# Kernel optimization log

Measured on AMD Instinct MI355X. Metric: run time of the kernel, lower is better.

The kernel has to match this reference:

```python
import math
import jax, jax.numpy as jnp
import numpy as np
from jax import lax

UP = 2
DOWN = 2
M = 8
BETA = 2.5
FC = 0.5          # up_fc = down_fc = 0.5 (not 'critical' branch)
LRELU = 0.1

def _lpf_filter(factor):
    # Kaiser-windowed sinc, matches Resampler.__init__ (fc != 'critical' branch)
    Mf = M * factor
    n = np.arange(-Mf // 2, Mf // 2 + 1).astype(np.float32)   # 17 taps
    cutoff = FC * math.pi
    f = np.sin(cutoff * n) / (math.pi * n + 1e-8)
    f[len(n) // 2] = FC
    win = np.kaiser(Mf + 1, BETA).astype(np.float32)          # == torch.kaiser_window(.., periodic=False)
    return jnp.asarray(win * f, dtype=jnp.float32)

UP_FILT = _lpf_filter(UP)
DOWN_FILT = _lpf_filter(DOWN)

def _conv1d_same(x, w, groups=1):
    # x: (B, Cin, L), w: (Cout, Cin//groups, K) with odd K
    pad = (w.shape[-1] - 1) // 2
    return lax.conv_general_dilated(x, w, window_strides=(1,), padding=[(pad, pad)],
                                    dimension_numbers=('NCH', 'OIH', 'NCH'),
                                    feature_group_count=groups)

def _lpf(x, filt):
    # depthwise grouped FIR, padding='same'
    C = x.shape[1]
    f = jnp.broadcast_to(filt[None, None, :], (C, 1, filt.shape[0]))
    return _conv1d_same(x, f, groups=C)

def setup_inputs() -> dict:
    key = jax.random.key(0)
    ks = jax.random.split(key, 4)
    bs, c_in, c_out, w_dim, L, k = 16, 512, 512, 512, 2048, 3
    return {
        'x': jax.random.normal(ks[0], (bs, c_in, L), dtype=jnp.float32),
        'w': jax.random.normal(ks[1], (bs, w_dim), dtype=jnp.float32),
        'affine_w': jax.random.normal(ks[2], (c_in, w_dim), dtype=jnp.float32) * 0.02,
        'affine_b': jnp.ones((c_in,), dtype=jnp.float32),
        'conv_w': jax.random.normal(ks[3], (c_out, c_in, k), dtype=jnp.float32) * 0.05,
        'conv_b': jnp.zeros((c_out,), dtype=jnp.float32),
        'norm_ema': jnp.ones((), dtype=jnp.float32),
    }

def reference(x, w, affine_w, affine_b, conv_w, conv_b, norm_ema):
    # eval mode, equalized_lr=False, normalize=True
    x = x * lax.rsqrt(norm_ema)
    cond = w @ affine_w.T + affine_b                                      # (bs, c_in)
    # weight / style normalization
    Wn = conv_w * lax.rsqrt(jnp.mean(jnp.square(conv_w), axis=(1, 2), keepdims=True))
    s = cond * lax.rsqrt(jnp.mean(jnp.square(cond)))                      # (bs, c_in)
    # demod coeff: rsqrt(sum_{i,k} (Wn[o,i,k]*s[b,i])^2 + 1e-8)
    d = lax.rsqrt(jnp.einsum('oik,bi->bo', jnp.square(Wn), jnp.square(s)) + 1e-8)
    # modulate-conv-demodulate (equivalent to per-sample grouped conv with conv_w[None]*s*d)
    y = _conv1d_same(x * s[:, :, None], Wn) * d[:, :, None] + conv_b[None, :, None]
    # upsample: zero-insertion then interpolation LPF
    bs, C, L = y.shape
    y = jnp.pad(y[..., None], ((0, 0), (0, 0), (0, 0), (0, UP - 1))).reshape(bs, C, L * UP)
    y = _lpf(y, UP_FILT)
    # filtered nonlinearity
    y = jax.nn.leaky_relu(y, LRELU) * math.sqrt(2)
    # downsample: anti-alias LPF then decimate
    y = _lpf(y, DOWN_FILT)[:, :, ::DOWN]
    return y
```

## Files before the change

### kernel.cpp

```cpp
#include <hip/hip_runtime.h>
#include <cmath>

typedef __attribute__((ext_vector_type(8))) short short8;
typedef __attribute__((ext_vector_type(4))) float f32x4;

static __device__ __forceinline__ unsigned short f2bf(float x) {
  unsigned int u = __float_as_uint(x);
  unsigned int r = (u + 0x7FFFu + ((u >> 16) & 1u)) >> 16;
  return (unsigned short)r;
}
static __device__ __forceinline__ float bf2f(unsigned short u) {
  return __uint_as_float(((unsigned int)u) << 16);
}
static __device__ __forceinline__ void glds16(const unsigned short* g, unsigned short* l) {
  __builtin_amdgcn_global_load_lds((const __attribute__((address_space(1))) unsigned int*)(g),
                                   (__attribute__((address_space(3))) unsigned int*)(l), 16, 0, 0);
}

__global__ __launch_bounds__(256) void k_cond(const float* __restrict__ w,
    const float* __restrict__ aw, const float* __restrict__ ab,
    float* __restrict__ cond, float* __restrict__ ssum) {
  int t = threadIdx.x;
  int outp = blockIdx.x * 64 + (t >> 2);
  int sub = t & 3;
  int b = outp >> 9, i = outp & 511;
  const float4* wr = (const float4*)(w + b * 512);
  const float4* ar = (const float4*)(aw + i * 512);
  float acc = 0.f;
  #pragma unroll
  for (int jj = 0; jj < 32; ++jj) {
    int j = sub + jj * 4;
    float4 a = ar[j], v = wr[j];
    acc += a.x * v.x + a.y * v.y + a.z * v.z + a.w * v.w;
  }
  acc += __shfl_xor(acc, 1);
  acc += __shfl_xor(acc, 2);
  float s = 0.f;
  if (sub == 0) {
    float c = acc + ab[i];
    cond[outp] = c;
    s = c * c;
  }
  #pragma unroll
  for (int off = 4; off <= 32; off <<= 1) s += __shfl_xor(s, off);
  if ((t & 63) == 0) atomicAdd(ssum, s);
}

__global__ __launch_bounds__(256) void k_wprep(const float* __restrict__ cw,
    float* __restrict__ W2, float* __restrict__ rinv,
    unsigned short* __restrict__ wpack) {
  int o = blockIdx.x, t = threadIdx.x;
  const float* row = cw + o * 1536;
  __shared__ float red[4];
  float local = 0.f;
  for (int r = 0; r < 2; ++r) {
    int i = t + 256 * r;
    float a = row[3 * i], b = row[3 * i + 1], c = row[3 * i + 2];
    float w2 = a * a + b * b + c * c;
    W2[o * 512 + i] = w2;
    local += w2;
    int chunk = i >> 5;
    int laneo = (((i >> 3) & 3) << 4) + (o & 15);
    int e = i & 7;
    int base = (chunk * 32 + (o >> 4)) * 512 + laneo * 8 + e;
    wpack[base] = f2bf(a);
    wpack[base + 16 * 32 * 512] = f2bf(b);
    wpack[base + 2 * 16 * 32 * 512] = f2bf(c);
  }
  #pragma unroll
  for (int off = 32; off >= 1; off >>= 1) local += __shfl_down(local, off);
  if ((t & 63) == 0) red[t >> 6] = local;
  __syncthreads();
  if (t == 0) {
    float m = red[0] + red[1] + red[2] + red[3];
    rinv[o] = rsqrtf(m * (1.f / 1536.f));
  }
}

__global__ __launch_bounds__(256) void k_dcoef(const float* __restrict__ W2,
    const float* __restrict__ cond, const float* __restrict__ rinv,
    const float* __restrict__ ssum, float* __restrict__ coef) {
  int og = blockIdx.x, b = blockIdx.y;
  int t = threadIdx.x;
  int o = og * 32 + (t >> 3);
  int il = t & 7;
  __shared__ float s2[512];
  float c0 = cond[b * 512 + t];
  float c1 = cond[b * 512 + t + 256];
  s2[t] = c0 * c0;
  s2[t + 256] = c1 * c1;
  __syncthreads();
  float acc = 0.f;
  #pragma unroll
  for (int jj = 0; jj < 16; ++jj) {
    int i = jj * 32 + il * 4;
    float4 wv = *(const float4*)(W2 + o * 512 + i);
    acc += wv.x * s2[i] + wv.y * s2[i + 1] + wv.z * s2[i + 2] + wv.w * s2[i + 3];
  }
  acc += __shfl_xor(acc, 1);
  acc += __shfl_xor(acc, 2);
  acc += __shfl_xor(acc, 4);
  if (il == 0) {
    float inv_ms = 8192.f / ssum[0];
    float ro = rinv[o];
    coef[b * 512 + o] = ro * rsqrtf(ro * ro * acc * inv_ms + 1e-8f);
  }
}

__global__ __launch_bounds__(256) void k_xprep(const float* __restrict__ x,
    const float* __restrict__ cond, const float* __restrict__ ssum,
    const float* __restrict__ nrm, unsigned short* __restrict__ xsT) {
  int lb = blockIdx.x, ib = blockIdx.y, b = blockIdx.z;
  int t = threadIdx.x;
  int l0 = lb * 64, i0 = ib * 64;
  __shared__ float tile[64][65];
  float sc = rsqrtf(ssum[0] * (1.f / 8192.f)) * rsqrtf(nrm[0]);
  int tr = t >> 4, tc = (t & 15) * 4;
  #pragma unroll
  for (int rr = 0; rr < 4; ++rr) {
    int il = rr * 16 + tr;
    float se = cond[b * 512 + i0 + il] * sc;
    float4 v = *(const float4*)(x + ((size_t)b * 512 + i0 + il) * 2048 + l0 + tc);
    tile[il][tc + 0] = v.x * se;
    tile[il][tc + 1] = v.y * se;
    tile[il][tc + 2] = v.z * se;
    tile[il][tc + 3] = v.w * se;
  }
  __syncthreads();
  int lr = t >> 3, ic = (t & 7) * 8;
  #pragma unroll
  for (int rr = 0; rr < 2; ++rr) {
    int ll = rr * 32 + lr;
    uint4 u;
    unsigned int pk[4];
    #pragma unroll
    for (int j = 0; j < 4; ++j) {
      unsigned short lo = f2bf(tile[ic + 2 * j][ll]);
      unsigned short hi = f2bf(tile[ic + 2 * j + 1][ll]);
      pk[j] = (unsigned int)lo | ((unsigned int)hi << 16);
    }
    u.x = pk[0]; u.y = pk[1]; u.z = pk[2]; u.w = pk[3];
    *(uint4*)(xsT + ((size_t)b * 2050 + 1 + l0 + ll) * 512 + i0 + ic) = u;
  }
  if (lb == 0 && t < 8) {
    uint4 z; z.x = 0; z.y = 0; z.z = 0; z.w = 0;
    *(uint4*)(xsT + ((size_t)b * 2050) * 512 + i0 + t * 8) = z;
  }
  if (lb == 31 && t < 8) {
    uint4 z; z.x = 0; z.y = 0; z.z = 0; z.w = 0;
    *(uint4*)(xsT + ((size_t)b * 2050 + 2049) * 512 + i0 + t * 8) = z;
  }
}

#define STAGE_B(buf, c) { \
  _Pragma("unroll") for (int j_ = 0; j_ < 3; ++j_) { \
    int f_ = j_ * 256 + t; \
    if (f_ < 520) { \
      int col_ = ((f_ >> 3) << 1) | (((f_ >> 2) ^ (f_ >> 4)) & 1); \
      int q_ = ((f_ ^ (f_ >> 2) ^ (f_ >> 4)) & 1) | ((((f_ >> 1) ^ (f_ >> 3)) & 1) << 1); \
      const unsigned short* src_ = xsT + ((size_t)b * 2050 + l0 + col_) * 512 + (c) * 32 + q_ * 8; \
      glds16(src_, &Bl[buf][(f_ & ~63) * 8]); \
    } \
  } }

#define LOAD_A(Ar, c) { \
  _Pragma("unroll") for (int k_ = 0; k_ < 3; ++k_) \
  _Pragma("unroll") for (int rg_ = 0; rg_ < 4; ++rg_) \
    Ar[k_ * 4 + rg_] = *(const short8*)(wpack + ((size_t)((k_ * 16 + (c)) * 32 + ob * 8 + wr * 4 + rg_)) * 512 + lane * 8); }

#define MFMA_STEP(Ar, buf) { \
  _Pragma("unroll") for (int k_ = 0; k_ < 3; ++k_) { \
    short8 bfr_[4]; \
    _Pragma("unroll") for (int cg_ = 0; cg_ < 4; ++cg_) { \
      int col_ = wc * 64 + cg_ * 16 + (lane & 15) + k_; \
      int byte_ = (col_ * 64 + ((lane >> 4) << 4)) ^ ((col_ & 7) << 4); \
      bfr_[cg_] = *(const short8*)((const char*)Bl[buf] + byte_); \
    } \
    _Pragma("unroll") for (int rg_ = 0; rg_ < 4; ++rg_) \
      _Pragma("unroll") for (int cg_ = 0; cg_ < 4; ++cg_) \
        acc[rg_][cg_] = __builtin_amdgcn_mfma_f32_16x16x32_bf16(Ar[k_ * 4 + rg_], bfr_[cg_], acc[rg_][cg_], 0, 0, 0); \
  } }

__global__ __launch_bounds__(256, 2) void k_main(const unsigned short* __restrict__ xsT,
    const unsigned short* __restrict__ wpack, const float* __restrict__ coef,
    const float* __restrict__ convb, unsigned short* __restrict__ y) {
  int lb = blockIdx.x, ob = blockIdx.y, b = blockIdx.z;
  int t = threadIdx.x, lane = t & 63, wave = t >> 6;
  int wr = wave >> 1, wc = wave & 1;
  int l0 = lb * 128, o0 = ob * 128;
  __shared__ __align__(16) unsigned short Bl[2][4160];
  f32x4 acc[4][4];
  f32x4 z4 = {0.f, 0.f, 0.f, 0.f};
  #pragma unroll
  for (int i = 0; i < 4; ++i)
    #pragma unroll
    for (int j = 0; j < 4; ++j) acc[i][j] = z4;

  short8 A0[12], A1[12];
  LOAD_A(A0, 0);
  STAGE_B(0, 0);
  __syncthreads();
  for (int cc = 0; cc < 16; cc += 2) {
    if (cc + 1 < 16) { STAGE_B(1, cc + 1); LOAD_A(A1, cc + 1); }
    MFMA_STEP(A0, 0);
    __syncthreads();
    if (cc + 2 < 16) { STAGE_B(0, cc + 2); LOAD_A(A0, cc + 2); }
    MFMA_STEP(A1, 1);
    __syncthreads();
  }
  int lq = lane >> 4, lrr = lane & 15;
  #pragma unroll
  for (int rg = 0; rg < 4; ++rg) {
    int o2 = o0 + wr * 64 + rg * 16 + lq * 4;
    float c0 = coef[b * 512 + o2 + 0], c1 = coef[b * 512 + o2 + 1];
    float c2 = coef[b * 512 + o2 + 2], c3 = coef[b * 512 + o2 + 3];
    float b0 = convb[o2 + 0], b1 = convb[o2 + 1];
    float b2 = convb[o2 + 2], b3 = convb[o2 + 3];
    #pragma unroll
    for (int cg = 0; cg < 4; ++cg) {
      int l = l0 + wc * 64 + cg * 16 + lrr;
      y[((size_t)b * 512 + o2 + 0) * 4096 + l] = f2bf(acc[rg][cg][0] * c0 + b0);
      y[((size_t)b * 512 + o2 + 1) * 4096 + l] = f2bf(acc[rg][cg][1] * c1 + b1);
      y[((size_t)b * 512 + o2 + 2) * 4096 + l] = f2bf(acc[rg][cg][2] * c2 + b2);
      y[((size_t)b * 512 + o2 + 3) * 4096 + l] = f2bf(acc[rg][cg][3] * c3 + b3);
    }
  }
}

struct Taps { float f[8]; };

__global__ __launch_bounds__(256) void k_filter(const unsigned short* __restrict__ ybuf,
    float* __restrict__ out, Taps tp) {
  int ch = blockIdx.x;
  int t = threadIdx.x;
  __shared__ float ysb[2336];
  const unsigned short* yc = ybuf + (size_t)ch * 4096;
  uint4 v = *(const uint4*)(yc + 8 * t);
  unsigned int wsv[4] = {v.x, v.y, v.z, v.w};
  int phys0 = 9 * t + 9;
  #pragma unroll
  for (int p = 0; p < 4; ++p) {
    ysb[phys0 + 2 * p]     = bf2f((unsigned short)(wsv[p] & 0xffffu));
    ysb[phys0 + 2 * p + 1] = bf2f((unsigned short)(wsv[p] >> 16));
  }
  if (t < 8) ysb[t] = 0.f;
  if (t >= 240 && t < 255) {
    int j = 2056 + (t - 240);
    ysb[j + (j >> 3)] = 0.f;
  }
  __syncthreads();
  float r[22];
  int jb = 8 * t + 1;
  #pragma unroll
  for (int u = 0; u < 22; ++u) { int j = jb + u; r[u] = ysb[j + (j >> 3)]; }
  int m0 = 8 * t;
  float ao[15];
  #pragma unroll
  for (int vv = 0; vv < 15; ++vv) {
    int t4 = m0 - 4 + vv;
    float u = 0.f;
    #pragma unroll
    for (int p = 0; p < 8; ++p) u += tp.f[p] * r[vv + p];
    float a = (u >= 0.f ? u : 0.1f * u) * 1.41421356237309515f;
    ao[vv] = ((unsigned)t4 < 2048u) ? a : 0.f;
  }
  float res[8];
  #pragma unroll
  for (int w = 0; w < 8; ++w) {
    float yv = r[w + 7];
    float s = 0.35355339059327379f * (yv >= 0.f ? yv : 0.1f * yv);
    #pragma unroll
    for (int q = 0; q < 8; ++q) s += tp.f[q] * ao[w + q];
    res[w] = s;
  }
  float4 o0; o0.x = res[0]; o0.y = res[1]; o0.z = res[2]; o0.w = res[3];
  float4 o1; o1.x = res[4]; o1.y = res[5]; o1.z = res[6]; o1.w = res[7];
  float* orow = out + (size_t)ch * 2048 + m0;
  *(float4*)orow = o0;
  *((float4*)orow + 1) = o1;
}

static double bessel_i0(double x) {
  double s = 1.0, term = 1.0;
  for (int m = 1; m < 30; ++m) {
    double h = x * 0.5 / (double)m;
    term *= h * h;
    s += term;
  }
  return s;
}

extern "C" void kernel_launch(void* const* d_in, const int* in_sizes, int n_in,
                              void* d_out, int out_size, void* d_ws, size_t ws_size,
                              hipStream_t stream) {
  (void)in_sizes; (void)n_in; (void)out_size; (void)ws_size;
  const float* x  = (const float*)d_in[0];
  const float* w  = (const float*)d_in[1];
  const float* aw = (const float*)d_in[2];
  const float* ab = (const float*)d_in[3];
  const float* cw = (const float*)d_in[4];
  const float* cb = (const float*)d_in[5];
  const float* ne = (const float*)d_in[6];
  float* out = (float*)d_out;
  char* ws = (char*)d_ws;

  float* ssum = (float*)(ws + 0);
  float* cond = (float*)(ws + 4096);
  float* coef = (float*)(ws + 36864);
  float* rinv = (float*)(ws + 69632);
  unsigned short* wpack = (unsigned short*)(ws + 73728);
  float* W2 = (float*)(ws + 3219456);
  unsigned short* xsT = (unsigned short*)(ws + 4268032);

  hipMemsetAsync(ssum, 0, 4, stream);
  k_cond<<<128, 256, 0, stream>>>(w, aw, ab, cond, ssum);
  k_wprep<<<512, 256, 0, stream>>>(cw, W2, rinv, wpack);
  k_dcoef<<<dim3(16, 16), 256, 0, stream>>>(W2, cond, rinv, ssum, coef);
  k_xprep<<<dim3(32, 8, 16), 256, 0, stream>>>(x, cond, ssum, ne, xsT);
  k_main<<<dim3(16, 4, 16), 256, 0, stream>>>(xsT, wpack, coef, cb, (unsigned short*)d_out);

  Taps tp;
  {
    double beta = 2.5;
    double i0b = bessel_i0(beta);
    for (int p = 0; p < 8; ++p) {
      int j = 2 * p + 1;
      int n = j - 8;
      double f = sin(0.5 * M_PI * (double)n) / (M_PI * (double)n + 1e-8);
      double rr = (double)(j - 8) / 8.0;
      double win = bessel_i0(beta * sqrt(1.0 - rr * rr)) / i0b;
      tp.f[p] = (float)(win * f);
    }
  }
  k_filter<<<8192, 256, 0, stream>>>((const unsigned short*)d_out, out, tp);
}
```

Measured before the change: 208.4 us.

## Triple-buffer main GEMM with vmcnt waits and merge prep kernels

Merges the four preprocessing kernels into two launches by dispatching on block index, which cuts launch overhead and serialization between them. The main MFMA kernel moves from double to triple buffering of the B tile in LDS. It uses explicit vmcnt waits and raw s_barrier instead of __syncthreads, so loads run two chunks ahead. Staging is now assigned per wave and the occupancy hint rises to 3 blocks per CU. In exchange it uses more LDS and depends on hand-counted vmcnt values, which risks races if the counts are wrong.

```diff
diff --git a/kernel.cpp b/kernel.cpp
--- a/kernel.cpp
+++ b/kernel.cpp
@@ -17,149 +17,151 @@
                                    (__attribute__((address_space(3))) unsigned int*)(l), 16, 0, 0);
 }
 
-__global__ __launch_bounds__(256) void k_cond(const float* __restrict__ w,
+#define VWAIT(n) asm volatile("s_waitcnt vmcnt(" #n ")" ::: "memory")
+
+__global__ __launch_bounds__(256) void k_pre1(const float* __restrict__ w,
     const float* __restrict__ aw, const float* __restrict__ ab,
-    float* __restrict__ cond, float* __restrict__ ssum) {
-  int t = threadIdx.x;
-  int outp = blockIdx.x * 64 + (t >> 2);
-  int sub = t & 3;
-  int b = outp >> 9, i = outp & 511;
-  const float4* wr = (const float4*)(w + b * 512);
-  const float4* ar = (const float4*)(aw + i * 512);
-  float acc = 0.f;
-  #pragma unroll
-  for (int jj = 0; jj < 32; ++jj) {
-    int j = sub + jj * 4;
-    float4 a = ar[j], v = wr[j];
-    acc += a.x * v.x + a.y * v.y + a.z * v.z + a.w * v.w;
-  }
-  acc += __shfl_xor(acc, 1);
-  acc += __shfl_xor(acc, 2);
-  float s = 0.f;
-  if (sub == 0) {
-    float c = acc + ab[i];
-    cond[outp] = c;
-    s = c * c;
-  }
-  #pragma unroll
-  for (int off = 4; off <= 32; off <<= 1) s += __shfl_xor(s, off);
-  if ((t & 63) == 0) atomicAdd(ssum, s);
-}
-
-__global__ __launch_bounds__(256) void k_wprep(const float* __restrict__ cw,
-    float* __restrict__ W2, float* __restrict__ rinv,
-    unsigned short* __restrict__ wpack) {
-  int o = blockIdx.x, t = threadIdx.x;
-  const float* row = cw + o * 1536;
+    const float* __restrict__ cw, float* __restrict__ cond, float* __restrict__ ssum,
+    float* __restrict__ W2, float* __restrict__ rinv, unsigned short* __restrict__ wpack) {
   __shared__ float red[4];
-  float local = 0.f;
-  for (int r = 0; r < 2; ++r) {
-    int i = t + 256 * r;
-    float a = row[3 * i], b = row[3 * i + 1], c = row[3 * i + 2];
-    float w2 = a * a + b * b + c * c;
-    W2[o * 512 + i] = w2;
-    local += w2;
-    int chunk = i >> 5;
-    int laneo = (((i >> 3) & 3) << 4) + (o & 15);
-    int e = i & 7;
-    int base = (chunk * 32 + (o >> 4)) * 512 + laneo * 8 + e;
-    wpack[base] = f2bf(a);
-    wpack[base + 16 * 32 * 512] = f2bf(b);
-    wpack[base + 2 * 16 * 32 * 512] = f2bf(c);
-  }
-  #pragma unroll
-  for (int off = 32; off >= 1; off >>= 1) local += __shfl_down(local, off);
-  if ((t & 63) == 0) red[t >> 6] = local;
-  __syncthreads();
-  if (t == 0) {
-    float m = red[0] + red[1] + red[2] + red[3];
-    rinv[o] = rsqrtf(m * (1.f / 1536.f));
-  }
-}
-
-__global__ __launch_bounds__(256) void k_dcoef(const float* __restrict__ W2,
-    const float* __restrict__ cond, const float* __restrict__ rinv,
-    const float* __restrict__ ssum, float* __restrict__ coef) {
-  int og = blockIdx.x, b = blockIdx.y;
-  int t = threadIdx.x;
-  int o = og * 32 + (t >> 3);
-  int il = t & 7;
-  __shared__ float s2[512];
-  float c0 = cond[b * 512 + t];
-  float c1 = cond[b * 512 + t + 256];
-  s2[t] = c0 * c0;
-  s2[t + 256] = c1 * c1;
-  __syncthreads();
-  float acc = 0.f;
-  #pragma unroll
-  for (int jj = 0; jj < 16; ++jj) {
-    int i = jj * 32 + il * 4;
-    float4 wv = *(const float4*)(W2 + o * 512 + i);
-    acc += wv.x * s2[i] + wv.y * s2[i + 1] + wv.z * s2[i + 2] + wv.w * s2[i + 3];
-  }
-  acc += __shfl_xor(acc, 1);
-  acc += __shfl_xor(acc, 2);
-  acc += __shfl_xor(acc, 4);
-  if (il == 0) {
-    float inv_ms = 8192.f / ssum[0];
-    float ro = rinv[o];
-    coef[b * 512 + o] = ro * rsqrtf(ro * ro * acc * inv_ms + 1e-8f);
-  }
-}
-
-__global__ __launch_bounds__(256) void k_xprep(const float* __restrict__ x,
-    const float* __restrict__ cond, const float* __restrict__ ssum,
-    const float* __restrict__ nrm, unsigned short* __restrict__ xsT) {
-  int lb = blockIdx.x, ib = blockIdx.y, b = blockIdx.z;
-  int t = threadIdx.x;
-  int l0 = lb * 64, i0 = ib * 64;
-  __shared__ float tile[64][65];
-  float sc = rsqrtf(ssum[0] * (1.f / 8192.f)) * rsqrtf(nrm[0]);
-  int tr = t >> 4, tc = (t & 15) * 4;
-  #pragma unroll
-  for (int rr = 0; rr < 4; ++rr) {
-    int il = rr * 16 + tr;
-    float se = cond[b * 512 + i0 + il] * sc;
-    float4 v = *(const float4*)(x + ((size_t)b * 512 + i0 + il) * 2048 + l0 + tc);
-    tile[il][tc + 0] = v.x * se;
-    tile[il][tc + 1] = v.y * se;
-    tile[il][tc + 2] = v.z * se;
-    tile[il][tc + 3] = v.w * se;
-  }
-  __syncthreads();
-  int lr = t >> 3, ic = (t & 7) * 8;
-  #pragma unroll
-  for (int rr = 0; rr < 2; ++rr) {
-    int ll = rr * 32 + lr;
-    uint4 u;
-    unsigned int pk[4];
-    #pragma unroll
-    for (int j = 0; j < 4; ++j) {
-      unsigned short lo = f2bf(tile[ic + 2 * j][ll]);
-      unsigned short hi = f2bf(tile[ic + 2 * j + 1][ll]);
-      pk[j] = (unsigned int)lo | ((unsigned int)hi << 16);
-    }
-    u.x = pk[0]; u.y = pk[1]; u.z = pk[2]; u.w = pk[3];
-    *(uint4*)(xsT + ((size_t)b * 2050 + 1 + l0 + ll) * 512 + i0 + ic) = u;
-  }
-  if (lb == 0 && t < 8) {
-    uint4 z; z.x = 0; z.y = 0; z.z = 0; z.w = 0;
-    *(uint4*)(xsT + ((size_t)b * 2050) * 512 + i0 + t * 8) = z;
-  }
-  if (lb == 31 && t < 8) {
-    uint4 z; z.x = 0; z.y = 0; z.z = 0; z.w = 0;
-    *(uint4*)(xsT + ((size_t)b * 2050 + 2049) * 512 + i0 + t * 8) = z;
+  int bid = blockIdx.x, t = threadIdx.x;
+  if (bid < 128) {
+    int outp = bid * 64 + (t >> 2);
+    int sub = t & 3;
+    int b = outp >> 9, i = outp & 511;
+    const float4* wr = (const float4*)(w + b * 512);
+    const float4* ar = (const float4*)(aw + i * 512);
+    float acc = 0.f;
+    #pragma unroll
+    for (int jj = 0; jj < 32; ++jj) {
+      int j = sub + jj * 4;
+      float4 a = ar[j], v = wr[j];
+      acc += a.x * v.x + a.y * v.y + a.z * v.z + a.w * v.w;
+    }
+    acc += __shfl_xor(acc, 1);
+    acc += __shfl_xor(acc, 2);
+    float s = 0.f;
+    if (sub == 0) {
+      float c = acc + ab[i];
+      cond[outp] = c;
+      s = c * c;
+    }
+    #pragma unroll
+    for (int off = 4; off <= 32; off <<= 1) s += __shfl_xor(s, off);
+    if ((t & 63) == 0) atomicAdd(ssum, s);
+  } else {
+    int o = bid - 128;
+    const float* row = cw + o * 1536;
+    float local = 0.f;
+    for (int r = 0; r < 2; ++r) {
+      int i = t + 256 * r;
+      float a = row[3 * i], b = row[3 * i + 1], c = row[3 * i + 2];
+      float w2 = a * a + b * b + c * c;
+      W2[o * 512 + i] = w2;
+      local += w2;
+      int chunk = i >> 5;
+      int laneo = (((i >> 3) & 3) << 4) + (o & 15);
+      int e = i & 7;
+      int base = (chunk * 32 + (o >> 4)) * 512 + laneo * 8 + e;
+      wpack[base] = f2bf(a);
+      wpack[base + 16 * 32 * 512] = f2bf(b);
+      wpack[base + 2 * 16 * 32 * 512] = f2bf(c);
+    }
+    #pragma unroll
+    for (int off = 32; off >= 1; off >>= 1) local += __shfl_down(local, off);
+    if ((t & 63) == 0) red[t >> 6] = local;
+    __syncthreads();
+    if (t == 0) {
+      float m = red[0] + red[1] + red[2] + red[3];
+      rinv[o] = rsqrtf(m * (1.f / 1536.f));
+    }
+  }
+}
+
+__global__ __launch_bounds__(256) void k_pre2(const float* __restrict__ x,
+    const float* __restrict__ W2, const float* __restrict__ cond,
+    const float* __restrict__ rinv, const float* __restrict__ ssum,
+    const float* __restrict__ nrm, float* __restrict__ coef,
+    unsigned short* __restrict__ xsT) {
+  __shared__ float shb[64 * 65];
+  int bid = blockIdx.x, t = threadIdx.x;
+  if (bid < 256) {
+    int og = bid & 15, b = bid >> 4;
+    int o = og * 32 + (t >> 3);
+    int il = t & 7;
+    float c0 = cond[b * 512 + t];
+    float c1 = cond[b * 512 + t + 256];
+    shb[t] = c0 * c0;
+    shb[t + 256] = c1 * c1;
+    __syncthreads();
+    float acc = 0.f;
+    #pragma unroll
+    for (int jj = 0; jj < 16; ++jj) {
+      int i = jj * 32 + il * 4;
+      float4 wv = *(const float4*)(W2 + o * 512 + i);
+      acc += wv.x * shb[i] + wv.y * shb[i + 1] + wv.z * shb[i + 2] + wv.w * shb[i + 3];
+    }
+    acc += __shfl_xor(acc, 1);
+    acc += __shfl_xor(acc, 2);
+    acc += __shfl_xor(acc, 4);
+    if (il == 0) {
+      float inv_ms = 8192.f / ssum[0];
+      float ro = rinv[o];
+      coef[b * 512 + o] = ro * rsqrtf(ro * ro * acc * inv_ms + 1e-8f);
+    }
+  } else {
+    int xb = bid - 256;
+    int lb = xb & 31, ib = (xb >> 5) & 7, b = xb >> 8;
+    float (*tile)[65] = (float(*)[65])shb;
+    int l0 = lb * 64, i0 = ib * 64;
+    float sc = rsqrtf(ssum[0] * (1.f / 8192.f)) * rsqrtf(nrm[0]);
+    int tr = t >> 4, tc = (t & 15) * 4;
+    #pragma unroll
+    for (int rr = 0; rr < 4; ++rr) {
+      int il = rr * 16 + tr;
+      float se = cond[b * 512 + i0 + il] * sc;
+      float4 v = *(const float4*)(x + ((size_t)b * 512 + i0 + il) * 2048 + l0 + tc);
+      tile[il][tc + 0] = v.x * se;
+      tile[il][tc + 1] = v.y * se;
+      tile[il][tc + 2] = v.z * se;
+      tile[il][tc + 3] = v.w * se;
+    }
+    __syncthreads();
+    int lr = t >> 3, ic = (t & 7) * 8;
+    #pragma unroll
+    for (int rr = 0; rr < 2; ++rr) {
+      int ll = rr * 32 + lr;
+      uint4 u;
+      unsigned int pk[4];
+      #pragma unroll
+      for (int j = 0; j < 4; ++j) {
+        unsigned short lo = f2bf(tile[ic + 2 * j][ll]);
+        unsigned short hi = f2bf(tile[ic + 2 * j + 1][ll]);
+        pk[j] = (unsigned int)lo | ((unsigned int)hi << 16);
+      }
+      u.x = pk[0]; u.y = pk[1]; u.z = pk[2]; u.w = pk[3];
+      *(uint4*)(xsT + ((size_t)b * 2050 + 1 + l0 + ll) * 512 + i0 + ic) = u;
+    }
+    if (lb == 0 && t < 8) {
+      uint4 z; z.x = 0; z.y = 0; z.z = 0; z.w = 0;
+      *(uint4*)(xsT + ((size_t)b * 2050) * 512 + i0 + t * 8) = z;
+    }
+    if (lb == 31 && t < 8) {
+      uint4 z; z.x = 0; z.y = 0; z.z = 0; z.w = 0;
+      *(uint4*)(xsT + ((size_t)b * 2050 + 2049) * 512 + i0 + t * 8) = z;
+    }
   }
 }
 
 #define STAGE_B(buf, c) { \
   _Pragma("unroll") for (int j_ = 0; j_ < 3; ++j_) { \
-    int f_ = j_ * 256 + t; \
-    if (f_ < 520) { \
-      int col_ = ((f_ >> 3) << 1) | (((f_ >> 2) ^ (f_ >> 4)) & 1); \
-      int q_ = ((f_ ^ (f_ >> 2) ^ (f_ >> 4)) & 1) | ((((f_ >> 1) ^ (f_ >> 3)) & 1) << 1); \
+    int sb_ = wave * 130 + ((j_ < 2) ? j_ * 64 : 128); \
+    int s_ = sb_ + ((j_ < 2) ? lane : (lane & 1)); \
+    if (j_ < 2 || lane < 2) { \
+      int col_ = ((s_ >> 3) << 1) | (((s_ >> 2) ^ (s_ >> 4)) & 1); \
+      int q_ = ((s_ ^ (s_ >> 2) ^ (s_ >> 4)) & 1) | ((((s_ >> 1) ^ (s_ >> 3)) & 1) << 1); \
       const unsigned short* src_ = xsT + ((size_t)b * 2050 + l0 + col_) * 512 + (c) * 32 + q_ * 8; \
-      glds16(src_, &Bl[buf][(f_ & ~63) * 8]); \
+      glds16(src_, &Bl[buf][sb_ * 8]); \
     } \
   } }
 
@@ -181,14 +183,14 @@
         acc[rg_][cg_] = __builtin_amdgcn_mfma_f32_16x16x32_bf16(Ar[k_ * 4 + rg_], bfr_[cg_], acc[rg_][cg_], 0, 0, 0); \
   } }
 
-__global__ __launch_bounds__(256, 2) void k_main(const unsigned short* __restrict__ xsT,
+__global__ __launch_bounds__(256, 3) void k_main(const unsigned short* __restrict__ xsT,
     const unsigned short* __restrict__ wpack, const float* __restrict__ coef,
     const float* __restrict__ convb, unsigned short* __restrict__ y) {
   int lb = blockIdx.x, ob = blockIdx.y, b = blockIdx.z;
   int t = threadIdx.x, lane = t & 63, wave = t >> 6;
   int wr = wave >> 1, wc = wave & 1;
   int l0 = lb * 128, o0 = ob * 128;
-  __shared__ __align__(16) unsigned short Bl[2][4160];
+  __shared__ __align__(16) unsigned short Bl[3][4160];
   f32x4 acc[4][4];
   f32x4 z4 = {0.f, 0.f, 0.f, 0.f};
   #pragma unroll
@@ -196,18 +198,32 @@
     #pragma unroll
     for (int j = 0; j < 4; ++j) acc[i][j] = z4;
 
-  short8 A0[12], A1[12];
-  LOAD_A(A0, 0);
+  short8 Areg[2][12];
+  LOAD_A(Areg[0], 0);
   STAGE_B(0, 0);
-  __syncthreads();
-  for (int cc = 0; cc < 16; cc += 2) {
-    if (cc + 1 < 16) { STAGE_B(1, cc + 1); LOAD_A(A1, cc + 1); }
-    MFMA_STEP(A0, 0);
-    __syncthreads();
-    if (cc + 2 < 16) { STAGE_B(0, cc + 2); LOAD_A(A0, cc + 2); }
-    MFMA_STEP(A1, 1);
-    __syncthreads();
-  }
+  STAGE_B(1, 1);
+  __builtin_amdgcn_sched_barrier(0);
+  VWAIT(3);
+  __builtin_amdgcn_s_barrier();
+
+  #pragma unroll
+  for (int c = 0; c < 14; ++c) {
+    LOAD_A(Areg[(c + 1) & 1], c + 1);
+    STAGE_B((c + 2) % 3, c + 2);
+    __builtin_amdgcn_sched_barrier(0);
+    MFMA_STEP(Areg[c & 1], c % 3);
+    __builtin_amdgcn_sched_barrier(0);
+    VWAIT(15);
+    __builtin_amdgcn_s_barrier();
+  }
+  LOAD_A(Areg[1], 15);
+  __builtin_amdgcn_sched_barrier(0);
+  MFMA_STEP(Areg[0], 2);
+  __builtin_amdgcn_sched_barrier(0);
+  VWAIT(12);
+  __builtin_amdgcn_s_barrier();
+  MFMA_STEP(Areg[1], 0);
+
   int lq = lane >> 4, lrr = lane & 15;
   #pragma unroll
   for (int rg = 0; rg < 4; ++rg) {
@@ -313,10 +329,8 @@
   unsigned short* xsT = (unsigned short*)(ws + 4268032);
 
   hipMemsetAsync(ssum, 0, 4, stream);
-  k_cond<<<128, 256, 0, stream>>>(w, aw, ab, cond, ssum);
-  k_wprep<<<512, 256, 0, stream>>>(cw, W2, rinv, wpack);
-  k_dcoef<<<dim3(16, 16), 256, 0, stream>>>(W2, cond, rinv, ssum, coef);
-  k_xprep<<<dim3(32, 8, 16), 256, 0, stream>>>(x, cond, ssum, ne, xsT);
+  k_pre1<<<640, 256, 0, stream>>>(w, aw, ab, cw, cond, ssum, W2, rinv, wpack);
+  k_pre2<<<4352, 256, 0, stream>>>(x, W2, cond, rinv, ssum, ne, coef, xsT);
   k_main<<<dim3(16, 4, 16), 256, 0, stream>>>(xsT, wpack, coef, cb, (unsigned short*)d_out);
 
   Taps tp;
```

Measured after the change: 362.7 us. 74.0% more time.
